# Kernel optimization log

Measured on AMD Instinct MI355X. Metric: run time of the kernel, lower is better.

## Reference

```python
import jax, jax.numpy as jnp
import numpy as np

N = 262144
K = 512          # num_knots
XMIN, XMAX = -3.0, 3.0
LN_EPS = 1e-5


def setup_inputs() -> dict:
    key = jax.random.key(0)
    k_x, k_w = jax.random.split(key)
    x = jax.random.normal(k_x, (N, 1), dtype=jnp.float32)
    # LayerNorm affine params (elementwise_affine=True init: gamma=1, beta=0)
    ln_gamma = jnp.ones((K,), dtype=jnp.float32)
    ln_beta = jnp.zeros((K,), dtype=jnp.float32)
    # head: Linear(K, 1), xavier_uniform with gain=2.0 -> bound = 2*sqrt(6/(K+1))
    bound = 2.0 * np.sqrt(6.0 / (K + 1))
    head_w = jax.random.uniform(k_w, (1, K), dtype=jnp.float32, minval=-bound, maxval=bound)
    head_b = jnp.zeros((1,), dtype=jnp.float32)
    return {"x": x, "ln_gamma": ln_gamma, "ln_beta": ln_beta,
            "head_w": head_w, "head_b": head_b}


def _cubic_bspline(t):
    # t: (N,) in [0,1) -> (N,4) cubic B-spline basis
    t2 = t * t
    t3 = t2 * t
    b0 = (1.0 - t) ** 3 / 6.0
    b1 = (3.0 * t3 - 6.0 * t2 + 4.0) / 6.0
    b2 = (-3.0 * t3 + 3.0 * t2 + 3.0 * t + 1.0) / 6.0
    b3 = t3 / 6.0
    return jnp.stack([b0, b1, b2, b3], axis=-1)


def _spline_features(x):
    # x: (N,1) -> feats: (N,K) via periodic cubic B-spline scatter
    x0 = (x - XMIN) / (XMAX - XMIN + 1e-8)
    u = jnp.remainder(x0 * K, K)          # (N,1), periodic wrap
    i = jnp.floor(u)
    frac = (u - i)[:, 0]                  # (N,)
    B = _cubic_bspline(frac)              # (N,4)
    base = i[:, 0].astype(jnp.int32)      # (N,)
    idx = jnp.remainder(base[:, None] + jnp.arange(4, dtype=jnp.int32)[None, :], K)  # (N,4)
    rows = jnp.arange(x.shape[0], dtype=jnp.int32)[:, None]
    feats = jnp.zeros((x.shape[0], K), dtype=x.dtype).at[rows, idx].add(B)
    return feats


def reference(x, ln_gamma, ln_beta, head_w, head_b):
    feats = _spline_features(x)                       # (N,K)
    mu = jnp.mean(feats, axis=-1, keepdims=True)
    var = jnp.mean((feats - mu) ** 2, axis=-1, keepdims=True)
    feats = (feats - mu) * jax.lax.rsqrt(var + LN_EPS) * ln_gamma + ln_beta
    return feats @ head_w.T + head_b                  # (N,1)
```

## Files before the change

### kernel.cpp

```cpp
#include <hip/hip_runtime.h>

#define K_KNOTS 512
#define NTHREADS 256

__device__ __forceinline__ float kan_one(float xs, const float* __restrict__ gw,
                                         float C1, float C2) {
    float x0 = (xs + 3.0f) / 6.0f;
    float u = x0 * 512.0f;
    u = fmodf(u, 512.0f);
    if (u < 0.0f) u += 512.0f;
    float fi = floorf(u);
    float t = u - fi;
    int base = (int)fi;

    float t2 = t * t;
    float t3 = t2 * t;
    float omt = 1.0f - t;
    float b0 = omt * omt * omt / 6.0f;
    float b1 = (3.0f * t3 - 6.0f * t2 + 4.0f) / 6.0f;
    float b2 = (-3.0f * t3 + 3.0f * t2 + 3.0f * t + 1.0f) / 6.0f;
    float b3 = t3 / 6.0f;

    float S = b0 + b1 + b2 + b3;
    float mu = S * (1.0f / 512.0f);
    float d0 = b0 - mu, d1 = b1 - mu, d2 = b2 - mu, d3 = b3 - mu;
    float var = (d0 * d0 + d1 * d1 + d2 * d2 + d3 * d3
                 + (512.0f - 4.0f) * (mu * mu)) * (1.0f / 512.0f);
    float rs = rsqrtf(var + 1e-5f);

    float g0 = gw[ base      & 511];
    float g1 = gw[(base + 1) & 511];
    float g2 = gw[(base + 2) & 511];
    float g3 = gw[(base + 3) & 511];
    float dot = b0 * g0 + b1 * g1 + b2 * g2 + b3 * g3;

    return rs * (dot - mu * C1) + C2;
}

__global__ __launch_bounds__(NTHREADS) void kan1d_fused(
    const float* __restrict__ x,
    const float* __restrict__ ln_gamma,
    const float* __restrict__ ln_beta,
    const float* __restrict__ head_w,
    const float* __restrict__ head_b,
    float* __restrict__ out,
    int n4, int n)
{
    __shared__ float gw[K_KNOTS];
    __shared__ float red[8];
    __shared__ float sC1, sC2;

    const int tid = threadIdx.x;

    float c1 = 0.0f, c2 = 0.0f;
    for (int k = tid; k < K_KNOTS; k += NTHREADS) {
        float g = ln_gamma[k];
        float w = head_w[k];
        float v = g * w;
        gw[k] = v;
        c1 += v;
        c2 += ln_beta[k] * w;
    }
#pragma unroll
    for (int off = 32; off > 0; off >>= 1) {
        c1 += __shfl_down(c1, off, 64);
        c2 += __shfl_down(c2, off, 64);
    }
    const int lane = tid & 63, wid = tid >> 6;
    if (lane == 0) { red[wid] = c1; red[4 + wid] = c2; }
    __syncthreads();
    if (tid == 0) {
        sC1 = red[0] + red[1] + red[2] + red[3];
        sC2 = red[4] + red[5] + red[6] + red[7] + head_b[0];
    }
    __syncthreads();
    const float C1 = sC1;
    const float C2 = sC2;

    const float4* __restrict__ xv4 = (const float4*)x;
    float4* __restrict__ ov4 = (float4*)out;

    for (int i = blockIdx.x * NTHREADS + tid; i < n4; i += gridDim.x * NTHREADS) {
        float4 xv = xv4[i];
        float4 yv;
        yv.x = kan_one(xv.x, gw, C1, C2);
        yv.y = kan_one(xv.y, gw, C1, C2);
        yv.z = kan_one(xv.z, gw, C1, C2);
        yv.w = kan_one(xv.w, gw, C1, C2);
        ov4[i] = yv;
    }
    for (int i = n4 * 4 + blockIdx.x * NTHREADS + tid; i < n;
         i += gridDim.x * NTHREADS) {
        out[i] = kan_one(x[i], gw, C1, C2);
    }
}

extern "C" void kernel_launch(void* const* d_in, const int* in_sizes, int n_in,
                              void* d_out, int out_size, void* d_ws, size_t ws_size,
                              hipStream_t stream) {
    const float* x        = (const float*)d_in[0];
    const float* ln_gamma = (const float*)d_in[1];
    const float* ln_beta  = (const float*)d_in[2];
    const float* head_w   = (const float*)d_in[3];
    const float* head_b   = (const float*)d_in[4];
    float* out = (float*)d_out;

    const int n = in_sizes[0];
    const int n4 = n >> 2;

    kan1d_fused<<<256, NTHREADS, 0, stream>>>(x, ln_gamma, ln_beta, head_w,
                                              head_b, out, n4, n);
}
```

Before: 62.76 us.

## Use one float4 per thread with full grid and early x load

```diff
diff --git a/kernel.cpp b/kernel.cpp
--- a/kernel.cpp
+++ b/kernel.cpp
@@ -6,26 +6,24 @@
 __device__ __forceinline__ float kan_one(float xs, const float* __restrict__ gw,
                                          float C1, float C2) {
     float x0 = (xs + 3.0f) / 6.0f;
-    float u = x0 * 512.0f;
-    u = fmodf(u, 512.0f);
-    if (u < 0.0f) u += 512.0f;
-    float fi = floorf(u);
-    float t = u - fi;
-    int base = (int)fi;
+    float w  = x0 * 512.0f;
+    float fw = floorf(w);
+    float t  = w - fw;
+    int base = (int)fw;
 
     float t2 = t * t;
     float t3 = t2 * t;
     float omt = 1.0f - t;
-    float b0 = omt * omt * omt / 6.0f;
-    float b1 = (3.0f * t3 - 6.0f * t2 + 4.0f) / 6.0f;
-    float b2 = (-3.0f * t3 + 3.0f * t2 + 3.0f * t + 1.0f) / 6.0f;
-    float b3 = t3 / 6.0f;
+    float b0 = omt * omt * omt * (1.0f / 6.0f);
+    float b1 = (3.0f * t3 - 6.0f * t2 + 4.0f) * (1.0f / 6.0f);
+    float b2 = (-3.0f * t3 + 3.0f * t2 + 3.0f * t + 1.0f) * (1.0f / 6.0f);
+    float b3 = t3 * (1.0f / 6.0f);
 
     float S = b0 + b1 + b2 + b3;
     float mu = S * (1.0f / 512.0f);
     float d0 = b0 - mu, d1 = b1 - mu, d2 = b2 - mu, d3 = b3 - mu;
     float var = (d0 * d0 + d1 * d1 + d2 * d2 + d3 * d3
-                 + (512.0f - 4.0f) * (mu * mu)) * (1.0f / 512.0f);
+                 + 508.0f * (mu * mu)) * (1.0f / 512.0f);
     float rs = rsqrtf(var + 1e-5f);
 
     float g0 = gw[ base      & 511];
@@ -51,15 +49,21 @@
     __shared__ float sC1, sC2;
 
     const int tid = threadIdx.x;
+    const int gi = blockIdx.x * NTHREADS + tid;
+
+    const float4* __restrict__ xv4 = (const float4*)x;
+    float4 xv;
+    const bool valid = gi < n4;
+    if (valid) xv = xv4[gi];
 
     float c1 = 0.0f, c2 = 0.0f;
     for (int k = tid; k < K_KNOTS; k += NTHREADS) {
         float g = ln_gamma[k];
-        float w = head_w[k];
-        float v = g * w;
+        float hw = head_w[k];
+        float v = g * hw;
         gw[k] = v;
         c1 += v;
-        c2 += ln_beta[k] * w;
+        c2 += ln_beta[k] * hw;
     }
 #pragma unroll
     for (int off = 32; off > 0; off >>= 1) {
@@ -77,20 +81,15 @@
     const float C1 = sC1;
     const float C2 = sC2;
 
-    const float4* __restrict__ xv4 = (const float4*)x;
-    float4* __restrict__ ov4 = (float4*)out;
-
-    for (int i = blockIdx.x * NTHREADS + tid; i < n4; i += gridDim.x * NTHREADS) {
-        float4 xv = xv4[i];
+    if (valid) {
         float4 yv;
         yv.x = kan_one(xv.x, gw, C1, C2);
         yv.y = kan_one(xv.y, gw, C1, C2);
         yv.z = kan_one(xv.z, gw, C1, C2);
         yv.w = kan_one(xv.w, gw, C1, C2);
-        ov4[i] = yv;
+        ((float4*)out)[gi] = yv;
     }
-    for (int i = n4 * 4 + blockIdx.x * NTHREADS + tid; i < n;
-         i += gridDim.x * NTHREADS) {
+    for (int i = n4 * 4 + gi; i < n; i += gridDim.x * NTHREADS) {
         out[i] = kan_one(x[i], gw, C1, C2);
     }
 }
@@ -107,7 +106,8 @@
 
     const int n = in_sizes[0];
     const int n4 = n >> 2;
+    const int nblocks = (n4 + NTHREADS - 1) / NTHREADS;
 
-    kan1d_fused<<<256, NTHREADS, 0, stream>>>(x, ln_gamma, ln_beta, head_w,
-                                              head_b, out, n4, n);
+    kan1d_fused<<<nblocks, NTHREADS, 0, stream>>>(x, ln_gamma, ln_beta, head_w,
+                                                  head_b, out, n4, n);
 }
```

Measured after the change: 62.03 us. About the same (-1.2%).
